# Kernel tuning notes

Hardware: AMD Instinct MI355X
Metric: run time of the kernel (lower is better)

The kernel has to match this reference:

```python
import jax, jax.numpy as jnp
import numpy as np

BATCH = 8192
INPUT_DIM = 10240
NODES = 1024          # == INPUT_DIM // 10, required by compressed @ adjacency
ACTIONS = 64
HIDDEN = 128
BINS = 100
HLO, HHI = -5.0, 5.0
ENTROPY_THRESH = 2.5


def _semantic_mask(n):
    m = np.zeros((n, n), dtype=np.float32)
    m[9, 0] = 1.0; m[9, 1] = 1.0; m[3, 0] = 1.0; m[2, 7] = 1.0; m[6, 4] = 1.0
    np.fill_diagonal(m, 1.0)
    m[8, 5] = 1.0; m[8, 1] = 1.0; m[8, 3] = 1.0
    if n > 6:
        m[5, 6] = 10.0
        m[1, 6] = 5.0
    if n > 5:
        m[5, 3] = 2.0
    return jnp.asarray(m)


def setup_inputs() -> dict:
    key = jax.random.key(0)
    ks = jax.random.split(key, 6)
    event_stream = jax.random.normal(ks[0], (BATCH, INPUT_DIM), dtype=jnp.float32)
    sensing_matrix = jax.random.normal(ks[1], (INPUT_DIM // 10, INPUT_DIM), dtype=jnp.float32)
    # adjacency is a trainable parameter (zeros at init); use small random values
    # so the downstream state/policy computation is non-degenerate.
    adjacency = 0.01 * jax.random.normal(ks[2], (NODES, NODES), dtype=jnp.float32)
    semantic_mask = _semantic_mask(NODES)
    W1 = jax.random.normal(ks[3], (HIDDEN, NODES), dtype=jnp.float32) / np.sqrt(NODES)
    b1 = jnp.zeros((HIDDEN,), dtype=jnp.float32)
    W2 = jax.random.normal(ks[4], (ACTIONS, HIDDEN), dtype=jnp.float32) / np.sqrt(HIDDEN)
    b2 = jnp.zeros((ACTIONS,), dtype=jnp.float32)
    return {"event_stream": event_stream, "sensing_matrix": sensing_matrix,
            "adjacency": adjacency, "semantic_mask": semantic_mask,
            "W1": W1, "b1": b1, "W2": W2, "b2": b2}


def _batched_histc(x):
    # Faithful vectorized torch.histc(bins=100, min=-5, max=5):
    # out-of-range values are ignored; values == max land in the last bin.
    b = x.shape[0]
    idx = jnp.clip(jnp.floor((x - HLO) / (HHI - HLO) * BINS).astype(jnp.int32), 0, BINS - 1)
    in_range = ((x >= HLO) & (x <= HHI)).astype(x.dtype)
    rows = jnp.broadcast_to(jnp.arange(b)[:, None], x.shape)
    return jnp.zeros((b, BINS), dtype=x.dtype).at[rows, idx].add(in_range)


def _policy(s, W1, b1, W2, b2):
    h = jax.nn.relu(s @ W1.T + b1)
    return h @ W2.T + b2


def reference(event_stream, sensing_matrix, adjacency, semantic_mask, W1, b1, W2, b2):
    # --- Layer 1: information filter (batched histogram + Shannon entropy gate) ---
    hist = _batched_histc(event_stream)                       # [B, 100]
    prob = hist / (hist.sum(-1, keepdims=True) + 1e-9)
    h_ent = -(prob * jnp.log(prob + 1e-9)).sum(-1)            # [B]
    compressed = event_stream @ sensing_matrix.T              # [B, NODES]
    keep = (h_ent >= ENTROPY_THRESH)[:, None].astype(compressed.dtype)
    filtered = compressed * keep                              # zeros where low entropy

    # --- Layer 2: causal forward ---
    state = filtered @ adjacency                              # [B, NODES]

    # --- Semantic consistency loss ---
    semantic_loss = jnp.sum(jnp.abs(adjacency) * semantic_mask)

    # --- Layer 3: robust Nash policy (training path: sign-grad perturbation) ---
    grad_s = jax.grad(lambda s: _policy(s, W1, b1, W2, b2).mean())(state)
    perturbation = jnp.sign(grad_s)
    robust_logits = _policy(state - 0.1 * perturbation, W1, b1, W2, b2)
    action_probs = jax.nn.softmax(robust_logits, axis=-1)     # [B, ACTIONS]

    return action_probs, adjacency, semantic_loss
```

## Files before the change

### kernel.cpp

```cpp
#include <hip/hip_runtime.h>
#include <hip/hip_bf16.h>

typedef unsigned short u16;
typedef short v8s __attribute__((ext_vector_type(8)));
typedef float v4f __attribute__((ext_vector_type(4)));

#define BATCH 8192
#define IND 10240
#define NODES 1024
#define ACTIONS 64
#define HIDDEN 128

__device__ __forceinline__ u16 f2b(float x) {
    __hip_bfloat16 h = __float2bfloat16(x);
    return *reinterpret_cast<u16*>(&h);
}

__device__ __forceinline__ float b2f(u16 x) {
    unsigned u = ((unsigned)x) << 16;
    return *reinterpret_cast<float*>(&u);
}

__device__ __forceinline__ void gload16(const void* g, void* l) {
    __builtin_amdgcn_global_load_lds(
        (const __attribute__((address_space(1))) void*)g,
        (__attribute__((address_space(3))) void*)l, 16, 0, 0);
}

#define SBAR() do { __builtin_amdgcn_s_barrier(); \
                    __builtin_amdgcn_sched_barrier(0); } while (0)
#define VMCNT4() asm volatile("s_waitcnt vmcnt(4)" ::: "memory")
#define VMCNT0() asm volatile("s_waitcnt vmcnt(0)" ::: "memory")

__global__ __launch_bounds__(256) void hist_entropy_cast(
    const float* __restrict__ E, u16* __restrict__ Ebf, float* __restrict__ keep)
{
    __shared__ int hist[4][100];
    const int tid = threadIdx.x;
    const int wave = tid >> 6;
    const int b = blockIdx.x;
    for (int j = tid; j < 400; j += 256) ((int*)hist)[j] = 0;
    __syncthreads();

    const float* row = E + (size_t)b * IND;
    u16* orow = Ebf + (size_t)b * IND;
    for (int i = tid * 4; i < IND; i += 1024) {
        float4 v = *reinterpret_cast<const float4*>(row + i);
        float xs[4] = {v.x, v.y, v.z, v.w};
        u16 ob[4];
#pragma unroll
        for (int j = 0; j < 4; ++j) {
            float x = xs[j];
            ob[j] = f2b(x);
            if (x >= -5.0f && x <= 5.0f) {
                int idx = (int)floorf((x + 5.0f) / 10.0f * 100.0f);
                idx = idx < 0 ? 0 : (idx > 99 ? 99 : idx);
                atomicAdd(&hist[wave][idx], 1);
            }
        }
        u16 packed[4] = {ob[0], ob[1], ob[2], ob[3]};
        *reinterpret_cast<uint2*>(orow + i) = *reinterpret_cast<uint2*>(packed);
    }
    __syncthreads();
    if (tid < 100)
        hist[0][tid] = hist[0][tid] + hist[1][tid] + hist[2][tid] + hist[3][tid];
    __syncthreads();

    if (tid < 64) {
        float c0 = (float)hist[0][tid];
        float c1 = (tid < 36) ? (float)hist[0][tid + 64] : 0.0f;
        float tot = c0 + c1;
#pragma unroll
        for (int s = 32; s >= 1; s >>= 1) tot += __shfl_xor(tot, s);
        float denom = tot + 1e-9f;
        float p0 = c0 / denom, p1 = c1 / denom;
        float e = -(p0 * logf(p0 + 1e-9f)) - (p1 * logf(p1 + 1e-9f));
#pragma unroll
        for (int s = 32; s >= 1; s >>= 1) e += __shfl_xor(e, s);
        if (tid == 0) keep[b] = (e >= 2.5f) ? 1.0f : 0.0f;
    }
}

__global__ __launch_bounds__(256) void cvt_bf16(
    const float* __restrict__ in, u16* __restrict__ out, long n4)
{
    long i = (long)blockIdx.x * blockDim.x + threadIdx.x;
    const long stride = (long)gridDim.x * blockDim.x;
    for (; i < n4; i += stride) {
        float4 v = reinterpret_cast<const float4*>(in)[i];
        u16 o[4] = {f2b(v.x), f2b(v.y), f2b(v.z), f2b(v.w)};
        reinterpret_cast<uint2*>(out)[i] = *reinterpret_cast<uint2*>(o);
    }
}

__global__ void transpose_cvt(const float* __restrict__ in, u16* __restrict__ out,
                              int R, int C)
{
    __shared__ float t[32][33];
    const int bx = blockIdx.x * 32, by = blockIdx.y * 32;
    const int tx = threadIdx.x, ty = threadIdx.y;
#pragma unroll
    for (int j = 0; j < 32; j += 8) {
        int r = by + ty + j, c = bx + tx;
        if (r < R && c < C) t[ty + j][tx] = in[(size_t)r * C + c];
    }
    __syncthreads();
#pragma unroll
    for (int j = 0; j < 32; j += 8) {
        int oc = by + tx;
        int orow = bx + ty + j;
        if (orow < C && oc < R) out[(size_t)orow * R + oc] = f2b(t[tx][ty + j]);
    }
}

__global__ void w2sum_k(const float* __restrict__ W2, float* __restrict__ w2s)
{
    int i = threadIdx.x;
    if (i < HIDDEN) {
        float s = 0.f;
        for (int a = 0; a < ACTIONS; ++a) s += W2[a * HIDDEN + i];
        w2s[i] = s;
    }
}

__global__ __launch_bounds__(256) void semloss1(
    const float* __restrict__ A, const float* __restrict__ M, float* __restrict__ part)
{
    const int tid = threadIdx.x;
    float s = 0.f;
    for (int i = blockIdx.x * 256 + tid; i < NODES * NODES; i += 256 * gridDim.x)
        s += fabsf(A[i]) * M[i];
    __shared__ float ws[4];
#pragma unroll
    for (int off = 32; off >= 1; off >>= 1) s += __shfl_xor(s, off);
    if ((tid & 63) == 0) ws[tid >> 6] = s;
    __syncthreads();
    if (tid == 0) part[blockIdx.x] = ws[0] + ws[1] + ws[2] + ws[3];
}

__global__ void semloss2(const float* __restrict__ part, float* __restrict__ out, int n)
{
    const int tid = threadIdx.x;
    float s = (tid < n) ? part[tid] : 0.f;
    __shared__ float ws[4];
#pragma unroll
    for (int off = 32; off >= 1; off >>= 1) s += __shfl_xor(s, off);
    if ((tid & 63) == 0) ws[tid >> 6] = s;
    __syncthreads();
    if (tid == 0) out[0] = ws[0] + ws[1] + ws[2] + ws[3];
}

__global__ __launch_bounds__(256) void combine_keep(
    const float* __restrict__ p0, const float* __restrict__ p1,
    const float* __restrict__ keep, u16* __restrict__ filt)
{
    long base = ((long)blockIdx.x * 256 + threadIdx.x) * 4;
    float4 a = *reinterpret_cast<const float4*>(p0 + base);
    float4 b = *reinterpret_cast<const float4*>(p1 + base);
    float k = keep[base >> 10];
    u16 o[4] = {f2b((a.x + b.x) * k), f2b((a.y + b.y) * k),
                f2b((a.z + b.z) * k), f2b((a.w + b.w) * k)};
    *reinterpret_cast<uint2*>(filt + base) = *reinterpret_cast<uint2*>(o);
}

__device__ __forceinline__ void stage_chunk(
    const u16* __restrict__ g, char* lds, int chunk_off, int kt_col,
    int tid, int wave)
{
    const int s_row0 = tid >> 2;
    const int gblk = (tid & 3) ^ ((tid >> 3) & 3);
#pragma unroll
    for (int j = 0; j < 2; ++j) {
        int lrow = j * 128 + s_row0;
        gload16(g + (size_t)lrow * IND + kt_col + (gblk << 3),
                lds + chunk_off + j * 8192 + (wave << 10));
    }
}

__global__ __launch_bounds__(512, 2) void gemm8_ep0(
    const u16* __restrict__ A, const u16* __restrict__ B,
    float* __restrict__ outf)
{
    extern __shared__ char lds[];
    const int tid = threadIdx.x;
    const int wave = tid >> 6, lane = tid & 63;
    const int wr = wave >> 2, wcn = wave & 3;
    const int l15 = lane & 15, lhi = lane >> 4;
    const int rsw = (lhi ^ ((l15 >> 1) & 3)) << 4;
    const size_t koff = (size_t)blockIdx.z * (IND / 2);
    const u16* Ag = A + (size_t)(blockIdx.x * 256) * IND + koff;
    const u16* Bg = B + (size_t)(blockIdx.y * 256) * IND + koff;

    v4f acc[8][4];
#pragma unroll
    for (int m = 0; m < 8; ++m)
#pragma unroll
        for (int n = 0; n < 4; ++n) acc[m][n] = (v4f){0.f, 0.f, 0.f, 0.f};

    v8s aq[4], bq[4];
    const int arow = wr * 128 * 64;
    const int brow0 = wcn * 64 * 64;

#define LDA(P, KS, M) (*reinterpret_cast<const v8s*>( \
    lds + ((P)*2 + (KS)) * 16384 + arow + ((M)*16 + l15) * 64 + rsw))
#define LDB(P, KS, NF) (*reinterpret_cast<const v8s*>( \
    lds + 65536 + ((P)*2 + (KS)) * 16384 + brow0 + ((NF)*16 + l15) * 64 + rsw))
#define QMFMA(MB) do { \
    _Pragma("unroll") \
    for (int m = 0; m < 4; ++m) \
        _Pragma("unroll") \
        for (int n = 0; n < 4; ++n) \
            acc[(MB) + m][n] = __builtin_amdgcn_mfma_f32_16x16x32_bf16( \
                aq[m], bq[n], acc[(MB) + m][n], 0, 0, 0); \
    } while (0)

#define TILE(P, KTN, STG) do { \
     \
    _Pragma("unroll") \
    for (int m = 0; m < 4; ++m) aq[m] = LDA(P, 0, m); \
    _Pragma("unroll") \
    for (int n = 0; n < 4; ++n) bq[n] = LDB(P, 0, n); \
    if (STG) stage_chunk(Ag, lds, ((P^1)*2 + 0) * 16384, (KTN), tid, wave); \
    SBAR(); \
    __builtin_amdgcn_s_setprio(1); QMFMA(0); __builtin_amdgcn_s_setprio(0); \
    SBAR(); \
     \
    _Pragma("unroll") \
    for (int m = 0; m < 4; ++m) aq[m] = LDA(P, 0, 4 + m); \
    if (STG) { stage_chunk(Bg, lds, 65536 + ((P^1)*2 + 0) * 16384, (KTN), tid, wave); \
               VMCNT4(); } else { VMCNT0(); } \
    SBAR(); \
    __builtin_amdgcn_s_setprio(1); QMFMA(4); __builtin_amdgcn_s_setprio(0); \
    SBAR(); \
     \
    _Pragma("unroll") \
    for (int m = 0; m < 4; ++m) aq[m] = LDA(P, 1, m); \
    _Pragma("unroll") \
    for (int n = 0; n < 4; ++n) bq[n] = LDB(P, 1, n); \
    if (STG) stage_chunk(Ag, lds, ((P^1)*2 + 1) * 16384, (KTN) + 32, tid, wave); \
    SBAR(); \
    __builtin_amdgcn_s_setprio(1); QMFMA(0); __builtin_amdgcn_s_setprio(0); \
    SBAR(); \
     \
    _Pragma("unroll") \
    for (int m = 0; m < 4; ++m) aq[m] = LDA(P, 1, 4 + m); \
    if (STG) { stage_chunk(Bg, lds, 65536 + ((P^1)*2 + 1) * 16384, (KTN) + 32, tid, wave); \
               VMCNT4(); } \
    SBAR(); \
    __builtin_amdgcn_s_setprio(1); QMFMA(4); __builtin_amdgcn_s_setprio(0); \
    SBAR(); \
} while (0)

    stage_chunk(Ag, lds, 0 * 16384, 0, tid, wave);
    stage_chunk(Bg, lds, 65536 + 0 * 16384, 0, tid, wave);
    stage_chunk(Ag, lds, 1 * 16384, 32, tid, wave);
    stage_chunk(Bg, lds, 65536 + 1 * 16384, 32, tid, wave);
    VMCNT4();
    SBAR();

#pragma unroll 1
    for (int tp = 0; tp < 39; ++tp) {
        TILE(0, (2 * tp + 1) * 64, 1);
        TILE(1, (2 * tp + 2) * 64, 1);
    }
    TILE(0, 79 * 64, 1);
    TILE(1, 0, 0);

#undef TILE
#undef QMFMA
#undef LDB
#undef LDA

    const size_t zo = (size_t)blockIdx.z * ((size_t)BATCH * NODES);
    const int grow0 = blockIdx.x * 256 + wr * 128 + (lhi << 2);
    const int gcol0 = blockIdx.y * 256 + wcn * 64 + l15;
#pragma unroll
    for (int m = 0; m < 8; ++m)
#pragma unroll
        for (int n = 0; n < 4; ++n)
#pragma unroll
            for (int j = 0; j < 4; ++j)
                outf[zo + (size_t)(grow0 + m * 16 + j) * NODES + gcol0 + n * 16] =
                    acc[m][n][j];
}

template<int EP>
__global__ __launch_bounds__(256) void gemm_bt(
    const u16* __restrict__ A, const u16* __restrict__ B, int K, int N,
    const float* __restrict__ aux0, const float* __restrict__ aux1,
    u16* __restrict__ outb)
{
    __shared__ u16 As[2][128 * 64];
    __shared__ u16 Bs[2][128 * 64];
    const int tid = threadIdx.x;
    const int wave = tid >> 6, lane = tid & 63;
    const int wr = wave >> 1, wc = wave & 1;
    const int l15 = lane & 15, lhi = lane >> 4;
    const int swz = (l15 & 7) << 3;
    const int src_c = (((lane & 7) ^ (lane >> 3)) << 3);
    const int src_r = lane >> 3;
    const u16* Ag = A + (size_t)(blockIdx.x * 128) * K;
    const u16* Bg = B + (size_t)(blockIdx.y * 128) * K;

    v4f acc[4][4];
#pragma unroll
    for (int m = 0; m < 4; ++m)
#pragma unroll
        for (int n = 0; n < 4; ++n) acc[m][n] = (v4f){0.f, 0.f, 0.f, 0.f};

#pragma unroll
    for (int i = 0; i < 4; ++i) {
        int chunk = wave * 4 + i;
        int r = chunk * 8 + src_r;
        gload16(Ag + (size_t)r * K + src_c, &As[0][chunk * 512]);
        gload16(Bg + (size_t)r * K + src_c, &Bs[0][chunk * 512]);
    }
    __syncthreads();

    int cur = 0;
    for (int kt = 0; kt < K; kt += 64) {
        if (kt + 64 < K) {
            int nxt = cur ^ 1;
#pragma unroll
            for (int i = 0; i < 4; ++i) {
                int chunk = wave * 4 + i;
                int r = chunk * 8 + src_r;
                gload16(Ag + (size_t)r * K + (kt + 64 + src_c), &As[nxt][chunk * 512]);
                gload16(Bg + (size_t)r * K + (kt + 64 + src_c), &Bs[nxt][chunk * 512]);
            }
        }
#pragma unroll
        for (int ks = 0; ks < 2; ++ks) {
            v8s a[4], b[4];
#pragma unroll
            for (int m = 0; m < 4; ++m)
                a[m] = *reinterpret_cast<const v8s*>(
                    &As[cur][(wr * 64 + m * 16 + l15) * 64 + ((ks * 32 + (lhi << 3)) ^ swz)]);
#pragma unroll
            for (int n = 0; n < 4; ++n)
                b[n] = *reinterpret_cast<const v8s*>(
                    &Bs[cur][(wc * 64 + n * 16 + l15) * 64 + ((ks * 32 + (lhi << 3)) ^ swz)]);
#pragma unroll
            for (int m = 0; m < 4; ++m)
#pragma unroll
                for (int n = 0; n < 4; ++n)
                    acc[m][n] = __builtin_amdgcn_mfma_f32_16x16x32_bf16(
                        a[m], b[n], acc[m][n], 0, 0, 0);
        }
        __syncthreads();
        cur ^= 1;
    }

    const int m0 = blockIdx.x * 128 + wr * 64;
    const int n0 = blockIdx.y * 128 + wc * 64;
#pragma unroll
    for (int m = 0; m < 4; ++m) {
#pragma unroll
        for (int j = 0; j < 4; ++j) {
            int row = m0 + m * 16 + (lhi << 2) + j;
#pragma unroll
            for (int n = 0; n < 4; ++n) {
                int col = n0 + n * 16 + l15;
                float v = acc[m][n][j];
                size_t off = (size_t)row * N + col;
                if (EP == 1) {
                    outb[off] = f2b(v);
                } else if (EP == 2) {
                    float h = v + aux0[col];
                    outb[off] = (h > 0.f) ? f2b(aux1[col]) : (u16)0;
                } else {
                    float sg = (v > 0.f) ? 1.f : ((v < 0.f) ? -1.f : 0.f);
                    float sv = b2f(((const u16*)aux0)[off]);
                    outb[off] = f2b(sv - 0.1f * sg);
                }
            }
        }
    }
}

__global__ __launch_bounds__(256) void policy_final(
    const u16* __restrict__ S2, const u16* __restrict__ W1b,
    const float* __restrict__ b1, const u16* __restrict__ W2b,
    const float* __restrict__ b2, float* __restrict__ probs)
{
    __shared__ u16 As[128 * 64];
    __shared__ u16 Bs[128 * 64];
    __shared__ u16 H2[128 * 128];
    const int tid = threadIdx.x;
    const int wave = tid >> 6, lane = tid & 63;
    const int wr = wave >> 1, wc = wave & 1;
    const int l15 = lane & 15, lhi = lane >> 4;
    const int swz = (l15 & 7) << 3;
    const int src_c = (((lane & 7) ^ (lane >> 3)) << 3);
    const int src_r = lane >> 3;
    const u16* Ag = S2 + (size_t)(blockIdx.x * 128) * NODES;

    v4f acc[4][4];
#pragma unroll
    for (int m = 0; m < 4; ++m)
#pragma unroll
        for (int n = 0; n < 4; ++n) acc[m][n] = (v4f){0.f, 0.f, 0.f, 0.f};

    for (int kt = 0; kt < NODES; kt += 64) {
#pragma unroll
        for (int i = 0; i < 4; ++i) {
            int chunk = wave * 4 + i;
            int r = chunk * 8 + src_r;
            gload16(Ag + (size_t)r * NODES + (kt + src_c), &As[chunk * 512]);
            gload16(W1b + (size_t)r * NODES + (kt + src_c), &Bs[chunk * 512]);
        }
        __syncthreads();
#pragma unroll
        for (int ks = 0; ks < 2; ++ks) {
            v8s a[4], b[4];
#pragma unroll
            for (int m = 0; m < 4; ++m)
                a[m] = *reinterpret_cast<const v8s*>(
                    &As[(wr * 64 + m * 16 + l15) * 64 + ((ks * 32 + (lhi << 3)) ^ swz)]);
#pragma unroll
            for (int n = 0; n < 4; ++n)
                b[n] = *reinterpret_cast<const v8s*>(
                    &Bs[(wc * 64 + n * 16 + l15) * 64 + ((ks * 32 + (lhi << 3)) ^ swz)]);
#pragma unroll
            for (int m = 0; m < 4; ++m)
#pragma unroll
                for (int n = 0; n < 4; ++n)
                    acc[m][n] = __builtin_amdgcn_mfma_f32_16x16x32_bf16(
                        a[m], b[n], acc[m][n], 0, 0, 0);
        }
        __syncthreads();
    }

#pragma unroll
    for (int m = 0; m < 4; ++m)
#pragma unroll
        for (int j = 0; j < 4; ++j) {
            int lrow = wr * 64 + m * 16 + (lhi << 2) + j;
#pragma unroll
            for (int n = 0; n < 4; ++n) {
                int col = wc * 64 + n * 16 + l15;
                float v = acc[m][n][j] + b1[col];
                H2[lrow * 128 + (col ^ ((lrow & 7) << 3))] = f2b(v > 0.f ? v : 0.f);
            }
        }
#pragma unroll
    for (int i = 0; i < 4; ++i) {
        int e = (tid + i * 256) * 8;
        int row = e >> 7, col = e & 127;
        int dst = (row << 7) | (col ^ ((row & 7) << 3));
        *reinterpret_cast<v8s*>(&Bs[dst]) = *reinterpret_cast<const v8s*>(&W2b[e]);
    }
    __syncthreads();

    v4f a2[2][4];
#pragma unroll
    for (int m = 0; m < 2; ++m)
#pragma unroll
        for (int n = 0; n < 4; ++n) a2[m][n] = (v4f){0.f, 0.f, 0.f, 0.f};
#pragma unroll
    for (int ks = 0; ks < 4; ++ks) {
        v8s af[2], bf[4];
#pragma unroll
        for (int m = 0; m < 2; ++m)
            af[m] = *reinterpret_cast<const v8s*>(
                &H2[(wave * 32 + m * 16 + l15) * 128 + ((ks * 32 + (lhi << 3)) ^ swz)]);
#pragma unroll
        for (int n = 0; n < 4; ++n)
            bf[n] = *reinterpret_cast<const v8s*>(
                &Bs[(n * 16 + l15) * 128 + ((ks * 32 + (lhi << 3)) ^ swz)]);
#pragma unroll
        for (int m = 0; m < 2; ++m)
#pragma unroll
            for (int n = 0; n < 4; ++n)
                a2[m][n] = __builtin_amdgcn_mfma_f32_16x16x32_bf16(
                    af[m], bf[n], a2[m][n], 0, 0, 0);
    }

#pragma unroll
    for (int m = 0; m < 2; ++m) {
#pragma unroll
        for (int j = 0; j < 4; ++j) {
            int lrow = wave * 32 + m * 16 + (lhi << 2) + j;
            float v[4];
#pragma unroll
            for (int n = 0; n < 4; ++n) v[n] = a2[m][n][j] + b2[n * 16 + l15];
            float mx = fmaxf(fmaxf(v[0], v[1]), fmaxf(v[2], v[3]));
#pragma unroll
            for (int s = 8; s >= 1; s >>= 1) mx = fmaxf(mx, __shfl_xor(mx, s));
            float e[4], sum = 0.f;
#pragma unroll
            for (int n = 0; n < 4; ++n) { e[n] = expf(v[n] - mx); sum += e[n]; }
#pragma unroll
            for (int s = 8; s >= 1; s >>= 1) sum += __shfl_xor(sum, s);
            float inv = 1.0f / sum;
            size_t base = (size_t)(blockIdx.x * 128 + lrow) * ACTIONS;
#pragma unroll
            for (int n = 0; n < 4; ++n) probs[base + n * 16 + l15] = e[n] * inv;
        }
    }
}

extern "C" void kernel_launch(void* const* d_in, const int* in_sizes, int n_in,
                              void* d_out, int out_size, void* d_ws, size_t ws_size,
                              hipStream_t stream)
{
    const float* E   = (const float*)d_in[0];
    const float* S   = (const float*)d_in[1];
    const float* Adj = (const float*)d_in[2];
    const float* Msk = (const float*)d_in[3];
    const float* W1  = (const float*)d_in[4];
    const float* b1  = (const float*)d_in[5];
    const float* W2  = (const float*)d_in[6];
    const float* b2  = (const float*)d_in[7];
    float* out = (float*)d_out;

    char* ws = (char*)d_ws;
    u16*  Ebf  = (u16*)  (ws + 0UL);
    u16*  Sbf  = (u16*)  (ws + 167772160UL);
    u16*  Atb  = (u16*)  (ws + 188743680UL);
    u16*  W1b  = (u16*)  (ws + 190840832UL);
    u16*  W1tb = (u16*)  (ws + 191102976UL);
    u16*  W2b  = (u16*)  (ws + 191365120UL);
    float* w2s = (float*)(ws + 191381504UL);
    float* keep= (float*)(ws + 191382016UL);
    float* part= (float*)(ws + 191414784UL);
    u16*  filt = (u16*)  (ws + 191415808UL);
    float* pbuf = (float*)(ws + 208193024UL);
    u16*  stb  = (u16*)  (ws + 208193024UL);
    u16*  dbuf = (u16*)  (ws + 224970240UL);
    u16*  s2   = (u16*)  (ws + 227067392UL);

    hipFuncSetAttribute((const void*)gemm8_ep0,
                        hipFuncAttributeMaxDynamicSharedMemorySize, 131072);

    dim3 tb(32, 8);
    hist_entropy_cast<<<8192, 256, 0, stream>>>(E, Ebf, keep);
    cvt_bf16<<<2048, 256, 0, stream>>>(S, Sbf, (long)NODES * IND / 4);
    cvt_bf16<<<128, 256, 0, stream>>>(W1, W1b, (long)HIDDEN * NODES / 4);
    cvt_bf16<<<8, 256, 0, stream>>>(W2, W2b, (long)ACTIONS * HIDDEN / 4);
    transpose_cvt<<<dim3(32, 32), tb, 0, stream>>>(Adj, Atb, NODES, NODES);
    transpose_cvt<<<dim3(32, 4),  tb, 0, stream>>>(W1, W1tb, HIDDEN, NODES);
    w2sum_k<<<1, 128, 0, stream>>>(W2, w2s);
    semloss1<<<256, 256, 0, stream>>>(Adj, Msk, part);
    semloss2<<<1, 256, 0, stream>>>(part, out + 524288 + 1048576, 256);
    hipMemcpyAsync(out + 524288, Adj, sizeof(float) * 1048576,
                   hipMemcpyDeviceToDevice, stream);

    gemm8_ep0<<<dim3(32, 4, 2), 512, 131072, stream>>>(Ebf, Sbf, pbuf);
    combine_keep<<<8192, 256, 0, stream>>>(pbuf, pbuf + (size_t)BATCH * NODES,
                                           keep, filt);
    gemm_bt<1><<<dim3(64, 8), 256, 0, stream>>>(filt, Atb, NODES, NODES,
                                                nullptr, nullptr, stb);
    gemm_bt<2><<<dim3(64, 1), 256, 0, stream>>>(stb, W1b, NODES, HIDDEN,
                                                b1, w2s, dbuf);
    gemm_bt<3><<<dim3(64, 8), 256, 0, stream>>>(dbuf, W1tb, HIDDEN, NODES,
                                                (const float*)stb, nullptr, s2);
    policy_final<<<64, 256, 0, stream>>>(s2, W1b, b1, W2b, b2, out);
}
```

Before: 389.7 us.

## Reuse split-K LDS-pipelined GEMM for adjacency product and drop pre-MFMA barriers

The large bf16 GEMM kernel is generalised over leading dimension and K-tile count. It now also computes filtered @ adjacency, with a 2-way split-K into fp32 partials followed by a combine pass that casts to bf16. This replaces the simpler 128x128 gemm_bt<1> kernel. Separately, the barrier before each MFMA group in the pipelined tile macro is removed to cut synchronisation stalls, which relies on the trailing barrier alone for LDS hazards. The new split-K path adds about 64MB of fp32 partial writes and an extra combine kernel.

```diff
diff --git a/kernel.cpp b/kernel.cpp
--- a/kernel.cpp
+++ b/kernel.cpp
@@ -150,21 +150,22 @@
     if (tid == 0) out[0] = ws[0] + ws[1] + ws[2] + ws[3];
 }
 
-__global__ __launch_bounds__(256) void combine_keep(
+template<int KEEP>
+__global__ __launch_bounds__(256) void combine_k(
     const float* __restrict__ p0, const float* __restrict__ p1,
-    const float* __restrict__ keep, u16* __restrict__ filt)
+    const float* __restrict__ keep, u16* __restrict__ outb)
 {
     long base = ((long)blockIdx.x * 256 + threadIdx.x) * 4;
     float4 a = *reinterpret_cast<const float4*>(p0 + base);
     float4 b = *reinterpret_cast<const float4*>(p1 + base);
-    float k = keep[base >> 10];
+    float k = KEEP ? keep[base >> 10] : 1.0f;
     u16 o[4] = {f2b((a.x + b.x) * k), f2b((a.y + b.y) * k),
                 f2b((a.z + b.z) * k), f2b((a.w + b.w) * k)};
-    *reinterpret_cast<uint2*>(filt + base) = *reinterpret_cast<uint2*>(o);
+    *reinterpret_cast<uint2*>(outb + base) = *reinterpret_cast<uint2*>(o);
 }
 
 __device__ __forceinline__ void stage_chunk(
-    const u16* __restrict__ g, char* lds, int chunk_off, int kt_col,
+    const u16* __restrict__ g, int ld, char* lds, int chunk_off, int kt_col,
     int tid, int wave)
 {
     const int s_row0 = tid >> 2;
@@ -172,14 +173,14 @@
 #pragma unroll
     for (int j = 0; j < 2; ++j) {
         int lrow = j * 128 + s_row0;
-        gload16(g + (size_t)lrow * IND + kt_col + (gblk << 3),
+        gload16(g + (size_t)lrow * ld + kt_col + (gblk << 3),
                 lds + chunk_off + j * 8192 + (wave << 10));
     }
 }
 
 __global__ __launch_bounds__(512, 2) void gemm8_ep0(
     const u16* __restrict__ A, const u16* __restrict__ B,
-    float* __restrict__ outf)
+    int ld, int nt, float* __restrict__ outf)
 {
     extern __shared__ char lds[];
     const int tid = threadIdx.x;
@@ -187,9 +188,9 @@
     const int wr = wave >> 2, wcn = wave & 3;
     const int l15 = lane & 15, lhi = lane >> 4;
     const int rsw = (lhi ^ ((l15 >> 1) & 3)) << 4;
-    const size_t koff = (size_t)blockIdx.z * (IND / 2);
-    const u16* Ag = A + (size_t)(blockIdx.x * 256) * IND + koff;
-    const u16* Bg = B + (size_t)(blockIdx.y * 256) * IND + koff;
+    const size_t koff = (size_t)blockIdx.z * ((size_t)nt * 64);
+    const u16* Ag = A + (size_t)(blockIdx.x * 256) * ld + koff;
+    const u16* Bg = B + (size_t)(blockIdx.y * 256) * ld + koff;
 
     v4f acc[8][4];
 #pragma unroll
@@ -220,16 +221,14 @@
     for (int m = 0; m < 4; ++m) aq[m] = LDA(P, 0, m); \
     _Pragma("unroll") \
     for (int n = 0; n < 4; ++n) bq[n] = LDB(P, 0, n); \
-    if (STG) stage_chunk(Ag, lds, ((P^1)*2 + 0) * 16384, (KTN), tid, wave); \
-    SBAR(); \
+    if (STG) stage_chunk(Ag, ld, lds, ((P^1)*2 + 0) * 16384, (KTN), tid, wave); \
     __builtin_amdgcn_s_setprio(1); QMFMA(0); __builtin_amdgcn_s_setprio(0); \
     SBAR(); \
      \
     _Pragma("unroll") \
     for (int m = 0; m < 4; ++m) aq[m] = LDA(P, 0, 4 + m); \
-    if (STG) { stage_chunk(Bg, lds, 65536 + ((P^1)*2 + 0) * 16384, (KTN), tid, wave); \
+    if (STG) { stage_chunk(Bg, ld, lds, 65536 + ((P^1)*2 + 0) * 16384, (KTN), tid, wave); \
                VMCNT4(); } else { VMCNT0(); } \
-    SBAR(); \
     __builtin_amdgcn_s_setprio(1); QMFMA(4); __builtin_amdgcn_s_setprio(0); \
     SBAR(); \
      \
@@ -237,33 +236,31 @@
     for (int m = 0; m < 4; ++m) aq[m] = LDA(P, 1, m); \
     _Pragma("unroll") \
     for (int n = 0; n < 4; ++n) bq[n] = LDB(P, 1, n); \
-    if (STG) stage_chunk(Ag, lds, ((P^1)*2 + 1) * 16384, (KTN) + 32, tid, wave); \
-    SBAR(); \
+    if (STG) stage_chunk(Ag, ld, lds, ((P^1)*2 + 1) * 16384, (KTN) + 32, tid, wave); \
     __builtin_amdgcn_s_setprio(1); QMFMA(0); __builtin_amdgcn_s_setprio(0); \
     SBAR(); \
      \
     _Pragma("unroll") \
     for (int m = 0; m < 4; ++m) aq[m] = LDA(P, 1, 4 + m); \
-    if (STG) { stage_chunk(Bg, lds, 65536 + ((P^1)*2 + 1) * 16384, (KTN) + 32, tid, wave); \
+    if (STG) { stage_chunk(Bg, ld, lds, 65536 + ((P^1)*2 + 1) * 16384, (KTN) + 32, tid, wave); \
                VMCNT4(); } \
-    SBAR(); \
     __builtin_amdgcn_s_setprio(1); QMFMA(4); __builtin_amdgcn_s_setprio(0); \
     SBAR(); \
 } while (0)
 
-    stage_chunk(Ag, lds, 0 * 16384, 0, tid, wave);
-    stage_chunk(Bg, lds, 65536 + 0 * 16384, 0, tid, wave);
-    stage_chunk(Ag, lds, 1 * 16384, 32, tid, wave);
-    stage_chunk(Bg, lds, 65536 + 1 * 16384, 32, tid, wave);
+    stage_chunk(Ag, ld, lds, 0 * 16384, 0, tid, wave);
+    stage_chunk(Bg, ld, lds, 65536 + 0 * 16384, 0, tid, wave);
+    stage_chunk(Ag, ld, lds, 1 * 16384, 32, tid, wave);
+    stage_chunk(Bg, ld, lds, 65536 + 1 * 16384, 32, tid, wave);
     VMCNT4();
     SBAR();
 
 #pragma unroll 1
-    for (int tp = 0; tp < 39; ++tp) {
+    for (int tp = 0; tp < (nt - 2) / 2; ++tp) {
         TILE(0, (2 * tp + 1) * 64, 1);
         TILE(1, (2 * tp + 2) * 64, 1);
     }
-    TILE(0, 79 * 64, 1);
+    TILE(0, (nt - 1) * 64, 1);
     TILE(1, 0, 0);
 
 #undef TILE
@@ -363,9 +360,7 @@
                 int col = n0 + n * 16 + l15;
                 float v = acc[m][n][j];
                 size_t off = (size_t)row * N + col;
-                if (EP == 1) {
-                    outb[off] = f2b(v);
-                } else if (EP == 2) {
+                if (EP == 2) {
                     float h = v + aux0[col];
                     outb[off] = (h > 0.f) ? f2b(aux1[col]) : (u16)0;
                 } else {
@@ -529,6 +524,7 @@
     u16*  stb  = (u16*)  (ws + 208193024UL);
     u16*  dbuf = (u16*)  (ws + 224970240UL);
     u16*  s2   = (u16*)  (ws + 227067392UL);
+    float* p2  = (float*)(ws + 0UL);
 
     hipFuncSetAttribute((const void*)gemm8_ep0,
                         hipFuncAttributeMaxDynamicSharedMemorySize, 131072);
@@ -546,11 +542,12 @@
     hipMemcpyAsync(out + 524288, Adj, sizeof(float) * 1048576,
                    hipMemcpyDeviceToDevice, stream);
 
-    gemm8_ep0<<<dim3(32, 4, 2), 512, 131072, stream>>>(Ebf, Sbf, pbuf);
-    combine_keep<<<8192, 256, 0, stream>>>(pbuf, pbuf + (size_t)BATCH * NODES,
+    gemm8_ep0<<<dim3(32, 4, 2), 512, 131072, stream>>>(Ebf, Sbf, IND, 80, pbuf);
+    combine_k<1><<<8192, 256, 0, stream>>>(pbuf, pbuf + (size_t)BATCH * NODES,
                                            keep, filt);
-    gemm_bt<1><<<dim3(64, 8), 256, 0, stream>>>(filt, Atb, NODES, NODES,
-                                                nullptr, nullptr, stb);
+    gemm8_ep0<<<dim3(32, 4, 2), 512, 131072, stream>>>(filt, Atb, NODES, 8, p2);
+    combine_k<0><<<8192, 256, 0, stream>>>(p2, p2 + (size_t)BATCH * NODES,
+                                           nullptr, stb);
     gemm_bt<2><<<dim3(64, 1), 256, 0, stream>>>(stb, W1b, NODES, HIDDEN,
                                                 b1, w2s, dbuf);
     gemm_bt<3><<<dim3(64, 8), 256, 0, stream>>>(dbuf, W1tb, HIDDEN, NODES,
```

Result: slower. 401.4 us (+3.0%).
